# Kernel optimization log

Measured on AMD Instinct MI355X. Metric: run time of the kernel, lower is better.

Reference implementation:

```python
import jax, jax.numpy as jnp
import numpy as np

WIN = 8     # sliding-chunk window size (Long2DSCSelfAttention default w=8)
HEADS = 8   # num_heads


def setup_inputs() -> dict:
    key = jax.random.key(0)
    ks = jax.random.split(key, 3)
    B, C, H, W = 4, 512, 64, 64
    x = jax.random.normal(ks[0], (B, C, H, W), jnp.float32)
    w_qkv = jax.random.normal(ks[1], (3 * C, C), jnp.float32) * 0.02
    b_qkv = jnp.zeros((3 * C,), jnp.float32)
    w_proj = jax.random.normal(ks[2], (C, C), jnp.float32) * 0.02
    b_proj = jnp.zeros((C,), jnp.float32)
    return {"x": x, "w_qkv": w_qkv, "b_qkv": b_qkv, "w_proj": w_proj, "b_proj": b_proj}


def _chunk(t, nh, nw, win):
    B, _, _, h, d = t.shape
    t = t.reshape(B, nh, win, nw, win, h, d)
    return t.transpose(0, 5, 1, 3, 2, 4, 6).reshape(B, h, nh, nw, win * win, d)


def reference(x, w_qkv, b_qkv, w_proj, b_proj):
    B, C, H, W = x.shape
    win, heads = WIN, HEADS
    d = C // heads
    nh, nw = H // win, W // win
    m = win * win  # tokens per chunk

    xf = x.transpose(0, 2, 3, 1)                      # [B,H,W,C]
    qkv = xf @ w_qkv.T + b_qkv                        # [B,H,W,3C]
    qkv = qkv.reshape(B, H, W, 3, heads, d)
    q = _chunk(qkv[..., 0, :, :], nh, nw, win)        # [B,h,nh,nw,m,d]
    k = _chunk(qkv[..., 1, :, :], nh, nw, win)
    v = _chunk(qkv[..., 2, :, :], nh, nw, win)

    # pad chunk grid by one chunk on each side; gather 3x3 chunk neighborhoods
    kp = jnp.pad(k, ((0, 0), (0, 0), (1, 1), (1, 1), (0, 0), (0, 0)))
    vp = jnp.pad(v, ((0, 0), (0, 0), (1, 1), (1, 1), (0, 0), (0, 0)))
    k9 = jnp.concatenate([kp[:, :, i:i + nh, j:j + nw] for i in range(3) for j in range(3)], axis=4)  # [B,h,nh,nw,9m,d]
    v9 = jnp.concatenate([vp[:, :, i:i + nh, j:j + nw] for i in range(3) for j in range(3)], axis=4)

    # validity mask for neighbor chunks at the image boundary
    valid = jnp.pad(jnp.ones((nh, nw), bool), ((1, 1), (1, 1)))
    vmask = jnp.concatenate(
        [jnp.repeat(valid[i:i + nh, j:j + nw][..., None], m, axis=-1) for i in range(3) for j in range(3)],
        axis=-1)                                      # [nh,nw,9m]

    scale = float(d) ** -0.5
    attn = jnp.einsum('bhxyqd,bhxykd->bhxyqk', q * scale, k9)      # [B,h,nh,nw,m,9m]
    neg = jnp.asarray(-1e9, attn.dtype)
    attn = jnp.where(vmask[None, None, :, :, None, :], attn, neg)
    attn = jax.nn.softmax(attn, axis=-1)
    out = jnp.einsum('bhxyqk,bhxykd->bhxyqd', attn, v9)            # [B,h,nh,nw,m,d]

    out = out.reshape(B, heads, nh, nw, win, win, d)
    out = out.transpose(0, 2, 4, 3, 5, 1, 6).reshape(B, H, W, C)
    out = out @ w_proj.T + b_proj
    return out.transpose(0, 3, 1, 2)                               # [B,C,H,W]
```

## Files before the change

kernel.cpp:

```cpp
#include <hip/hip_runtime.h>
#include <cstdint>
#include <cstddef>

namespace {

constexpr int kC = 512;
constexpr int kHW = 4096;
constexpr int kHeads = 8;
constexpr int kChunkElems = 64 * 64;

typedef float f32x4 __attribute__((ext_vector_type(4)));
typedef _Float16 f16x8 __attribute__((ext_vector_type(8)));
union FragU { uint4 u; f16x8 h; };

__device__ __forceinline__ ushort f16rn(float x) {
  _Float16 h = (_Float16)x;
  ushort u;
  __builtin_memcpy(&u, &h, 2);
  return u;
}
__device__ __forceinline__ uint pack2(ushort a, ushort b) {
  return (uint)a | ((uint)b << 16);
}
__device__ __forceinline__ float fexp2(float x) {
  return exp2f(x);
}
__device__ __forceinline__ uint pkrtz(float a, float b) {
  auto h = __builtin_amdgcn_cvt_pkrtz(a, b);
  uint u;
  __builtin_memcpy(&u, &h, 4);
  return u;
}
__device__ __forceinline__ void gld16(const void* g, void* lds) {
  __builtin_amdgcn_global_load_lds(
      (const __attribute__((address_space(1))) uint32_t*)g,
      (__attribute__((address_space(3))) uint32_t*)lds, 16, 0, 0);
}

__global__ __launch_bounds__(256)
void convw16_kernel(const float* __restrict__ wqkv, ushort* __restrict__ wqh,
                    const float* __restrict__ wproj, ushort* __restrict__ wph)
{
  const int bx = blockIdx.x;
  const float* src;
  ushort* dst;
  int idx;
  if (bx < 384) { src = wqkv; dst = wqh; idx = (bx * 256 + threadIdx.x) * 8; }
  else { src = wproj; dst = wph; idx = ((bx - 384) * 256 + threadIdx.x) * 8; }
  float4 v0 = *(const float4*)(src + idx);
  float4 v1 = *(const float4*)(src + idx + 4);
  float xs[8] = {v0.x, v0.y, v0.z, v0.w, v1.x, v1.y, v1.z, v1.w};
  ushort hh[8];
#pragma unroll
  for (int e = 0; e < 8; ++e) hh[e] = f16rn(xs[e]);
  *(uint4*)(dst + idx) = make_uint4(pack2(hh[0], hh[1]), pack2(hh[2], hh[3]),
                                    pack2(hh[4], hh[5]), pack2(hh[6], hh[7]));
}

__global__ __launch_bounds__(256)
void convx_kernel(const float* __restrict__ x, ushort* __restrict__ xt)
{
  __shared__ float LT[64][68];
  const int tid = threadIdx.x;
  const int t0 = blockIdx.x * 64;
  const int c0 = blockIdx.y * 64;
  const int b  = blockIdx.z;
  const float* xb = x + (size_t)b * kC * kHW;

#pragma unroll
  for (int u = 0; u < 4; ++u) {
    int idx = tid + u * 256;
    int rc = idx >> 4;
    int t4 = (idx & 15) << 2;
    float4 val = *(const float4*)(xb + (size_t)(c0 + rc) * kHW + t0 + t4);
    LT[t4 + 0][rc] = val.x;
    LT[t4 + 1][rc] = val.y;
    LT[t4 + 2][rc] = val.z;
    LT[t4 + 3][rc] = val.w;
  }
  __syncthreads();
#pragma unroll
  for (int u = 0; u < 4; ++u) {
    int idx = tid + u * 256;
    int rt = idx >> 4;
    int c4 = (idx & 15) << 2;
    float4 v = *(const float4*)&LT[rt][c4];
    size_t o = ((size_t)b * kHW + t0 + rt) * kC + c0 + c4;
    *(ushort4*)(xt + o) = make_ushort4(f16rn(v.x), f16rn(v.y),
                                       f16rn(v.z), f16rn(v.w));
  }
}

__global__ __launch_bounds__(256)
void qkv_mfma_kernel(const ushort* __restrict__ xt,
                     const ushort* __restrict__ wq,
                     const float* __restrict__ bqkv,
                     ushort* __restrict__ qo, ushort* __restrict__ ko,
                     ushort* __restrict__ vo)
{
  __shared__ __align__(16) ushort As[128 * 64];
  __shared__ __align__(16) ushort Bs[128 * 64];

  const int tid  = threadIdx.x;
  const int lane = tid & 63;
  const int wv   = tid >> 6;
  const int quad = lane >> 4;
  const int l15  = lane & 15;
  const int wm = wv & 1, wn = wv >> 1;
  const int m0 = blockIdx.x * 128;
  const int n0 = blockIdx.y * 128;
  const int b  = blockIdx.z;

  const ushort* xb = xt + (size_t)b * kHW * kC;

  auto stage = [&](int k0) {
#pragma unroll
    for (int ii = 0; ii < 4; ++ii) {
      int i = wv * 4 + ii;
      int m = i * 8 + (lane >> 3);
      int gch = (lane & 7) ^ (m & 7);
      gld16(xb + (size_t)(m0 + m) * kC + k0 + gch * 8, (char*)As + i * 1024);
      gld16(wq + (size_t)(n0 + m) * kC + k0 + gch * 8, (char*)Bs + i * 1024);
    }
  };

  f32x4 acc[4][4];
#pragma unroll
  for (int i = 0; i < 4; ++i)
#pragma unroll
    for (int j = 0; j < 4; ++j) acc[i][j] = (f32x4){0.f, 0.f, 0.f, 0.f};

  stage(0);

  for (int kt = 0; kt < 8; ++kt) {
    asm volatile("s_waitcnt vmcnt(0)" ::: "memory");
    asm volatile("s_barrier" ::: "memory");

    FragU a0[4], a1[4], b0[4], b1[4];
#pragma unroll
    for (int mi = 0; mi < 4; ++mi) {
      int mr = wm * 64 + mi * 16 + l15;
      int sw = mr & 7;
      a0[mi].u = *(const uint4*)&As[mr * 64 + ((quad ^ sw) * 8)];
      a1[mi].u = *(const uint4*)&As[mr * 64 + (((4 + quad) ^ sw) * 8)];
    }
#pragma unroll
    for (int ni = 0; ni < 4; ++ni) {
      int nr = wn * 64 + ni * 16 + l15;
      int sw = nr & 7;
      b0[ni].u = *(const uint4*)&Bs[nr * 64 + ((quad ^ sw) * 8)];
      b1[ni].u = *(const uint4*)&Bs[nr * 64 + (((4 + quad) ^ sw) * 8)];
    }
    asm volatile("s_waitcnt lgkmcnt(0)" ::: "memory");
    asm volatile("s_barrier" ::: "memory");

    if (kt < 7) stage((kt + 1) * 64);

#pragma unroll
    for (int mi = 0; mi < 4; ++mi)
#pragma unroll
      for (int ni = 0; ni < 4; ++ni)
        acc[mi][ni] = __builtin_amdgcn_mfma_f32_16x16x32_f16(a0[mi].h, b0[ni].h, acc[mi][ni], 0, 0, 0);
#pragma unroll
    for (int mi = 0; mi < 4; ++mi)
#pragma unroll
      for (int ni = 0; ni < 4; ++ni)
        acc[mi][ni] = __builtin_amdgcn_mfma_f32_16x16x32_f16(a1[mi].h, b1[ni].h, acc[mi][ni], 0, 0, 0);
  }

  const int sec = n0 >> 9;
  const int jwbase = n0 + wn * 64;
  const int head = (jwbase >> 6) & 7;
  const size_t hbb = ((size_t)b * kHeads + head) * 64;
  float biasv[4];
#pragma unroll
  for (int ni = 0; ni < 4; ++ni) biasv[ni] = bqkv[jwbase + ni * 16 + l15];

  if (sec == 2) {
#pragma unroll
    for (int ni = 0; ni < 4; ++ni) {
      int dd = ni * 16 + l15;
#pragma unroll
      for (int mi = 0; mi < 4; ++mi) {
        int t0t = m0 + wm * 64 + mi * 16 + quad * 4;
        int h = t0t >> 6, w = t0t & 63;
        int cy = h >> 3, iy = h & 7, cx = w >> 3, ix = w & 7;
        size_t cb = (hbb + cy * 8 + cx) * (size_t)kChunkElems;
        int tokb = iy * 8 + ix;
        ushort hh[4];
#pragma unroll
        for (int r = 0; r < 4; ++r) hh[r] = f16rn(acc[mi][ni][r] + biasv[ni]);
        *(ushort4*)(vo + cb + (size_t)dd * 64 + tokb) = make_ushort4(hh[0], hh[1], hh[2], hh[3]);
      }
    }
  } else {
    ushort* dst = (sec == 0) ? qo : ko;
    const float sc = (sec == 0) ? 0.125f * 1.44269504089f : 1.0f;
    ushort* tH = As + wv * 1152;
    const int ltok = lane >> 2;
    const int dd0 = (lane & 3) * 16;
#pragma unroll
    for (int mi = 0; mi < 4; ++mi) {
#pragma unroll
      for (int ni = 0; ni < 4; ++ni)
#pragma unroll
        for (int r = 0; r < 4; ++r)
          tH[(quad * 4 + r) * 68 + ni * 16 + l15] =
              f16rn((acc[mi][ni][r] + biasv[ni]) * sc);
      int tg = m0 + wm * 64 + mi * 16 + ltok;
      int h = tg >> 6, w = tg & 63;
      int cy = h >> 3, iy = h & 7, cx = w >> 3, ix = w & 7;
      size_t cb = (hbb + cy * 8 + cx) * (size_t)kChunkElems
                + (size_t)(iy * 8 + ix) * 64 + dd0;
      uint4 h0 = *(const uint4*)&tH[ltok * 68 + dd0];
      uint4 h1 = *(const uint4*)&tH[ltok * 68 + dd0 + 8];
      *(uint4*)(dst + cb) = h0;
      *(uint4*)(dst + cb + 8) = h1;
    }
  }
}

__global__ __launch_bounds__(256)
void attn_mfma_kernel(const ushort* __restrict__ qg, const ushort* __restrict__ kg,
                      const ushort* __restrict__ vg,
                      ushort* __restrict__ ao)
{
  __shared__ __align__(16) ushort KB[4096], VB[4096];
  __shared__ __align__(16) ushort Ps[4 * 16 * 72];

  const int tid  = threadIdx.x;
  const int lane = tid & 63;
  const int wv   = tid >> 6;
  const int quad = lane >> 4;
  const int l15  = lane & 15;

  const int bx = blockIdx.x;
  const int g  = (bx & 7) * 4 + ((bx >> 3) >> 6);
  const int c  = (bx >> 3) & 63;
  const int b = g >> 3, head = g & 7;
  const int cy = c >> 3, cx = c & 7;

  const size_t hb = (size_t)b * kHeads + head;
  const size_t gbase = hb * 64 * (size_t)kChunkElems;
  const size_t cbase = gbase + (size_t)c * (size_t)kChunkElems;

  FragU aQ0, aQ1;
  {
    const ushort* qr = qg + cbase + (size_t)(wv * 16 + l15) * 64 + quad * 8;
    aQ0.u = *(const uint4*)(qr);
    aQ1.u = *(const uint4*)(qr + 32);
  }

  const int boff = ((lane >> 3) * 64) + (((lane & 7) ^ (lane >> 3)) * 8);
  const ushort* kgB = kg + gbase + boff + (size_t)(wv * 2) * 512;
  const ushort* vgB = vg + gbase + boff + (size_t)(wv * 2) * 512;
  char* kDst0 = (char*)KB + (wv * 2) * 1024;
  char* vDst0 = (char*)VB + (wv * 2) * 1024;

  int kvOff0[4], kvOff1[4];
  {
    const int sw = l15 & 7;
#pragma unroll
    for (int nt = 0; nt < 4; ++nt) {
      int row = nt * 16 + l15;
      kvOff0[nt] = row * 64 + ((quad ^ sw) * 8);
      kvOff1[nt] = row * 64 + (((4 + quad) ^ sw) * 8);
    }
  }

  ushort* PsW = Ps + wv * 1152;
  ushort* pWr = PsW + l15 * 72 + quad * 4;
  const ushort* pRd = PsW + l15 * 72 + quad * 8;

  unsigned long long list = 0ull;
  int cnt = 0;
#pragma unroll
  for (int p = 0; p < 9; ++p) {
    const int dy = p / 3 - 1, dx = p % 3 - 1;
    int ny = cy + dy, nx = cx + dx;
    if ((unsigned)ny < 8u && (unsigned)nx < 8u) {
      list |= (unsigned long long)(ny * 8 + nx) << (6 * cnt);
      ++cnt;
    }
  }

  f32x4 o[4];
#pragma unroll
  for (int r = 0; r < 4; ++r) o[r] = (f32x4){0.f, 0.f, 0.f, 0.f};
  float rsum = 0.f;

  {
    int ch0 = (int)(list & 63);
    const ushort* pk = kgB + (size_t)ch0 * kChunkElems;
    gld16(pk, kDst0);
    gld16(pk + 512, kDst0 + 1024);
    const ushort* pv = vgB + (size_t)ch0 * kChunkElems;
    gld16(pv, vDst0);
    gld16(pv + 512, vDst0 + 1024);
  }

  for (int i = 0; i < cnt; ++i) {
    const bool more = (i + 1 < cnt);
    const int chn = (int)((list >> (6 * (i + 1))) & 63);

    asm volatile("s_waitcnt vmcnt(2)" ::: "memory");
    asm volatile("s_barrier" ::: "memory");

    FragU kf[8];
#pragma unroll
    for (int nt = 0; nt < 4; ++nt) {
      kf[nt * 2].u     = *(const uint4*)&KB[kvOff0[nt]];
      kf[nt * 2 + 1].u = *(const uint4*)&KB[kvOff1[nt]];
    }
    asm volatile("s_waitcnt lgkmcnt(0)" ::: "memory");
    asm volatile("s_waitcnt vmcnt(0)" ::: "memory");
    asm volatile("s_barrier" ::: "memory");

    if (more) {
      const ushort* pk = kgB + (size_t)chn * kChunkElems;
      gld16(pk, kDst0);
      gld16(pk + 512, kDst0 + 1024);
    }

    f32x4 s[4];
#pragma unroll
    for (int nt = 0; nt < 4; ++nt) s[nt] = (f32x4){0.f, 0.f, 0.f, 0.f};
#pragma unroll
    for (int nt = 0; nt < 4; ++nt) {
      s[nt] = __builtin_amdgcn_mfma_f32_16x16x32_f16(kf[nt * 2].h, aQ0.h, s[nt], 0, 0, 0);
      s[nt] = __builtin_amdgcn_mfma_f32_16x16x32_f16(kf[nt * 2 + 1].h, aQ1.h, s[nt], 0, 0, 0);
    }

#pragma unroll
    for (int nt = 0; nt < 4; ++nt) {
      float e0 = fexp2(s[nt][0]);
      float e1 = fexp2(s[nt][1]);
      float e2 = fexp2(s[nt][2]);
      float e3 = fexp2(s[nt][3]);
      rsum += (e0 + e1) + (e2 + e3);
      *(uint2*)(pWr + nt * 16) = make_uint2(pkrtz(e0, e1), pkrtz(e2, e3));
    }

    FragU aP0, aP1;
    aP0.u = *(const uint4*)(pRd);
    aP1.u = *(const uint4*)(pRd + 32);

#pragma unroll
    for (int nt = 0; nt < 4; ++nt) {
      FragU v0, v1;
      v0.u = *(const uint4*)&VB[kvOff0[nt]];
      v1.u = *(const uint4*)&VB[kvOff1[nt]];
      o[nt] = __builtin_amdgcn_mfma_f32_16x16x32_f16(v0.h, aP0.h, o[nt], 0, 0, 0);
      o[nt] = __builtin_amdgcn_mfma_f32_16x16x32_f16(v1.h, aP1.h, o[nt], 0, 0, 0);
    }

    asm volatile("s_waitcnt lgkmcnt(0)" ::: "memory");
    asm volatile("s_barrier" ::: "memory");
    if (more) {
      const ushort* pv = vgB + (size_t)chn * kChunkElems;
      gld16(pv, vDst0);
      gld16(pv + 512, vDst0 + 1024);
    }
  }

  rsum += __shfl_xor(rsum, 16, 64);
  rsum += __shfl_xor(rsum, 32, 64);
  const float inv = 1.0f / rsum;

  const int trg = wv * 16 + l15;
  const int hp = cy * 8 + (trg >> 3);
  const int wp = cx * 8 + (trg & 7);
  const size_t obase = ((size_t)b * kHW + hp * 64 + wp) * (size_t)kC + head * 64;

#pragma unroll
  for (int nt = 0; nt < 4; ++nt) {
    float v0 = o[nt][0] * inv;
    float v1 = o[nt][1] * inv;
    float v2 = o[nt][2] * inv;
    float v3 = o[nt][3] * inv;
    *(ushort4*)(ao + obase + nt * 16 + quad * 4) =
        make_ushort4(f16rn(v0), f16rn(v1), f16rn(v2), f16rn(v3));
  }
}

__global__ __launch_bounds__(256)
void proj_mfma_kernel(const ushort* __restrict__ ao,
                      const ushort* __restrict__ wp,
                      const float* __restrict__ bproj,
                      float* __restrict__ out)
{
  __shared__ __align__(16) ushort As[128 * 64];
  __shared__ __align__(16) ushort Bs[128 * 64];

  const int tid  = threadIdx.x;
  const int lane = tid & 63;
  const int wv   = tid >> 6;
  const int quad = lane >> 4;
  const int l15  = lane & 15;
  const int wm = wv & 1, wn = wv >> 1;
  const int n0g = blockIdx.x * 128;
  const int m0  = blockIdx.y * 128;
  const int b   = n0g >> 12;
  const int tl0 = n0g & 4095;

  auto stage = [&](int k0) {
#pragma unroll
    for (int ii = 0; ii < 4; ++ii) {
      int i = wv * 4 + ii;
      int m = i * 8 + (lane >> 3);
      int gch = (lane & 7) ^ (m & 7);
      gld16(wp + (size_t)(m0 + m) * kC + k0 + gch * 8, (char*)As + i * 1024);
      gld16(ao + (size_t)(n0g + m) * kC + k0 + gch * 8, (char*)Bs + i * 1024);
    }
  };

  f32x4 acc[4][4];
#pragma unroll
  for (int i = 0; i < 4; ++i)
#pragma unroll
    for (int j = 0; j < 4; ++j) acc[i][j] = (f32x4){0.f, 0.f, 0.f, 0.f};

  stage(0);

  for (int kt = 0; kt < 8; ++kt) {
    asm volatile("s_waitcnt vmcnt(0)" ::: "memory");
    asm volatile("s_barrier" ::: "memory");

    FragU a0[4], a1[4], b0[4], b1[4];
#pragma unroll
    for (int mi = 0; mi < 4; ++mi) {
      int mr = wm * 64 + mi * 16 + l15;
      int sw = mr & 7;
      a0[mi].u = *(const uint4*)&As[mr * 64 + ((quad ^ sw) * 8)];
      a1[mi].u = *(const uint4*)&As[mr * 64 + (((4 + quad) ^ sw) * 8)];
    }
#pragma unroll
    for (int ni = 0; ni < 4; ++ni) {
      int nr = wn * 64 + ni * 16 + l15;
      int sw = nr & 7;
      b0[ni].u = *(const uint4*)&Bs[nr * 64 + ((quad ^ sw) * 8)];
      b1[ni].u = *(const uint4*)&Bs[nr * 64 + (((4 + quad) ^ sw) * 8)];
    }
    asm volatile("s_waitcnt lgkmcnt(0)" ::: "memory");
    asm volatile("s_barrier" ::: "memory");

    if (kt < 7) stage((kt + 1) * 64);

#pragma unroll
    for (int mi = 0; mi < 4; ++mi)
#pragma unroll
      for (int ni = 0; ni < 4; ++ni)
        acc[mi][ni] = __builtin_amdgcn_mfma_f32_16x16x32_f16(a0[mi].h, b0[ni].h, acc[mi][ni], 0, 0, 0);
#pragma unroll
    for (int mi = 0; mi < 4; ++mi)
#pragma unroll
      for (int ni = 0; ni < 4; ++ni)
        acc[mi][ni] = __builtin_amdgcn_mfma_f32_16x16x32_f16(a1[mi].h, b1[ni].h, acc[mi][ni], 0, 0, 0);
  }

#pragma unroll
  for (int mi = 0; mi < 4; ++mi)
#pragma unroll
    for (int r = 0; r < 4; ++r) {
      int c = m0 + wm * 64 + mi * 16 + quad * 4 + r;
      float bias = bproj[c];
      size_t rowb = ((size_t)b * kC + c) * (size_t)kHW + tl0 + wn * 64;
#pragma unroll
      for (int ni = 0; ni < 4; ++ni)
        out[rowb + ni * 16 + l15] = acc[mi][ni][r] + bias;
    }
}

}

extern "C" void kernel_launch(void* const* d_in, const int* in_sizes, int n_in,
                              void* d_out, int out_size, void* d_ws, size_t ws_size,
                              hipStream_t stream)
{
  const float* x     = (const float*)d_in[0];
  const float* wqkv  = (const float*)d_in[1];
  const float* bqkv  = (const float*)d_in[2];
  const float* wproj = (const float*)d_in[3];
  const float* bproj = (const float*)d_in[4];
  float* out = (float*)d_out;

  const size_t seg = (size_t)2048 * kChunkElems;
  ushort* base = (ushort*)d_ws;
  ushort* qb = base + 0 * seg;
  ushort* kb = base + 1 * seg;
  ushort* vb = base + 2 * seg;
  ushort* xt = base + 3 * seg;
  ushort* ao = xt;
  ushort* wp16 = base + 4 * seg;
  ushort* wqh = base + 5 * seg;

  convw16_kernel<<<dim3(512), 256, 0, stream>>>(wqkv, wqh, wproj, wp16);
  convx_kernel<<<dim3(64, 8, 4), 256, 0, stream>>>(x, xt);
  qkv_mfma_kernel<<<dim3(32, 12, 4), 256, 0, stream>>>(xt, wqh, bqkv,
                                                       qb, kb, vb);
  attn_mfma_kernel<<<dim3(2048), 256, 0, stream>>>(qb, kb, vb, ao);
  proj_mfma_kernel<<<dim3(128, 4), 256, 0, stream>>>(ao, wp16, bproj, out);
}
```

Measured before the change: 176.9 us.

## Switch attention kernel to 32x32x16 MFMA tiles with 2x2 wave split

Reworks the attention kernel so each wave computes a 32-query by 32-key tile with 32x32x16 MFMA instructions instead of 16x16x32, splitting waves across query and key halves. P is shared through a block-wide LDS buffer and needs an extra barrier each chunk, and row sums are combined across waves through a small LDS array at the end. This halves the K fragment loads per wave and uses fewer, larger MFMAs, at the cost of added synchronisation and cross-wave dependencies in the P·V stage.

```diff
diff --git a/kernel.cpp b/kernel.cpp
--- a/kernel.cpp
+++ b/kernel.cpp
@@ -10,6 +10,7 @@
 constexpr int kChunkElems = 64 * 64;
 
 typedef float f32x4 __attribute__((ext_vector_type(4)));
+typedef float f32x16 __attribute__((ext_vector_type(16)));
 typedef _Float16 f16x8 __attribute__((ext_vector_type(8)));
 union FragU { uint4 u; f16x8 h; };
 
@@ -226,13 +227,16 @@
                       ushort* __restrict__ ao)
 {
   __shared__ __align__(16) ushort KB[4096], VB[4096];
-  __shared__ __align__(16) ushort Ps[4 * 16 * 72];
+  __shared__ __align__(16) ushort Ps[64 * 72];
+  __shared__ __align__(16) float  RsF[128];
 
   const int tid  = threadIdx.x;
   const int lane = tid & 63;
   const int wv   = tid >> 6;
-  const int quad = lane >> 4;
-  const int l15  = lane & 15;
+  const int l31  = lane & 31;
+  const int hi   = lane >> 5;
+  const int kq   = wv & 1;
+  const int qq   = wv >> 1;
 
   const int bx = blockIdx.x;
   const int g  = (bx & 7) * 4 + ((bx >> 3) >> 6);
@@ -244,11 +248,11 @@
   const size_t gbase = hb * 64 * (size_t)kChunkElems;
   const size_t cbase = gbase + (size_t)c * (size_t)kChunkElems;
 
-  FragU aQ0, aQ1;
+  FragU qf[4];
   {
-    const ushort* qr = qg + cbase + (size_t)(wv * 16 + l15) * 64 + quad * 8;
-    aQ0.u = *(const uint4*)(qr);
-    aQ1.u = *(const uint4*)(qr + 32);
+    const ushort* qr = qg + cbase + (size_t)(qq * 32 + l31) * 64 + hi * 8;
+#pragma unroll
+    for (int s = 0; s < 4; ++s) qf[s].u = *(const uint4*)(qr + s * 16);
   }
 
   const int boff = ((lane >> 3) * 64) + (((lane & 7) ^ (lane >> 3)) * 8);
@@ -257,20 +261,17 @@
   char* kDst0 = (char*)KB + (wv * 2) * 1024;
   char* vDst0 = (char*)VB + (wv * 2) * 1024;
 
-  int kvOff0[4], kvOff1[4];
+  int kvOff[4];
   {
-    const int sw = l15 & 7;
-#pragma unroll
-    for (int nt = 0; nt < 4; ++nt) {
-      int row = nt * 16 + l15;
-      kvOff0[nt] = row * 64 + ((quad ^ sw) * 8);
-      kvOff1[nt] = row * 64 + (((4 + quad) ^ sw) * 8);
-    }
-  }
-
-  ushort* PsW = Ps + wv * 1152;
-  ushort* pWr = PsW + l15 * 72 + quad * 4;
-  const ushort* pRd = PsW + l15 * 72 + quad * 8;
+    const int row = kq * 32 + l31;
+    const int sw = l31 & 7;
+#pragma unroll
+    for (int s = 0; s < 4; ++s)
+      kvOff[s] = row * 64 + (((2 * s + hi) ^ sw) * 8);
+  }
+
+  ushort* pWr = Ps + (qq * 32 + l31) * 72 + kq * 32 + 4 * hi;
+  const ushort* pRd = Ps + (qq * 32 + l31) * 72 + hi * 8;
 
   unsigned long long list = 0ull;
   int cnt = 0;
@@ -284,9 +285,9 @@
     }
   }
 
-  f32x4 o[4];
-#pragma unroll
-  for (int r = 0; r < 4; ++r) o[r] = (f32x4){0.f, 0.f, 0.f, 0.f};
+  f32x16 o32;
+#pragma unroll
+  for (int r = 0; r < 16; ++r) o32[r] = 0.f;
   float rsum = 0.f;
 
   {
@@ -306,12 +307,9 @@
     asm volatile("s_waitcnt vmcnt(2)" ::: "memory");
     asm volatile("s_barrier" ::: "memory");
 
-    FragU kf[8];
-#pragma unroll
-    for (int nt = 0; nt < 4; ++nt) {
-      kf[nt * 2].u     = *(const uint4*)&KB[kvOff0[nt]];
-      kf[nt * 2 + 1].u = *(const uint4*)&KB[kvOff1[nt]];
-    }
+    FragU kf[4];
+#pragma unroll
+    for (int s = 0; s < 4; ++s) kf[s].u = *(const uint4*)&KB[kvOff[s]];
     asm volatile("s_waitcnt lgkmcnt(0)" ::: "memory");
     asm volatile("s_waitcnt vmcnt(0)" ::: "memory");
     asm volatile("s_barrier" ::: "memory");
@@ -322,36 +320,32 @@
       gld16(pk + 512, kDst0 + 1024);
     }
 
-    f32x4 s[4];
-#pragma unroll
-    for (int nt = 0; nt < 4; ++nt) s[nt] = (f32x4){0.f, 0.f, 0.f, 0.f};
-#pragma unroll
-    for (int nt = 0; nt < 4; ++nt) {
-      s[nt] = __builtin_amdgcn_mfma_f32_16x16x32_f16(kf[nt * 2].h, aQ0.h, s[nt], 0, 0, 0);
-      s[nt] = __builtin_amdgcn_mfma_f32_16x16x32_f16(kf[nt * 2 + 1].h, aQ1.h, s[nt], 0, 0, 0);
-    }
-
-#pragma unroll
-    for (int nt = 0; nt < 4; ++nt) {
-      float e0 = fexp2(s[nt][0]);
-      float e1 = fexp2(s[nt][1]);
-      float e2 = fexp2(s[nt][2]);
-      float e3 = fexp2(s[nt][3]);
-      rsum += (e0 + e1) + (e2 + e3);
-      *(uint2*)(pWr + nt * 16) = make_uint2(pkrtz(e0, e1), pkrtz(e2, e3));
-    }
-
-    FragU aP0, aP1;
-    aP0.u = *(const uint4*)(pRd);
-    aP1.u = *(const uint4*)(pRd + 32);
-
-#pragma unroll
-    for (int nt = 0; nt < 4; ++nt) {
-      FragU v0, v1;
-      v0.u = *(const uint4*)&VB[kvOff0[nt]];
-      v1.u = *(const uint4*)&VB[kvOff1[nt]];
-      o[nt] = __builtin_amdgcn_mfma_f32_16x16x32_f16(v0.h, aP0.h, o[nt], 0, 0, 0);
-      o[nt] = __builtin_amdgcn_mfma_f32_16x16x32_f16(v1.h, aP1.h, o[nt], 0, 0, 0);
+    f32x16 s32;
+#pragma unroll
+    for (int r = 0; r < 16; ++r) s32[r] = 0.f;
+#pragma unroll
+    for (int s = 0; s < 4; ++s)
+      s32 = __builtin_amdgcn_mfma_f32_32x32x16_f16(kf[s].h, qf[s].h, s32, 0, 0, 0);
+
+    float e[16];
+#pragma unroll
+    for (int r = 0; r < 16; ++r) e[r] = fexp2(s32[r]);
+#pragma unroll
+    for (int r = 0; r < 16; ++r) rsum += e[r];
+#pragma unroll
+    for (int gg = 0; gg < 4; ++gg)
+      *(uint2*)(pWr + gg * 8) =
+          make_uint2(pkrtz(e[4 * gg], e[4 * gg + 1]),
+                     pkrtz(e[4 * gg + 2], e[4 * gg + 3]));
+    asm volatile("s_waitcnt lgkmcnt(0)" ::: "memory");
+    asm volatile("s_barrier" ::: "memory");
+
+#pragma unroll
+    for (int s = 0; s < 4; ++s) {
+      FragU vf, pf;
+      vf.u = *(const uint4*)&VB[kvOff[s]];
+      pf.u = *(const uint4*)(pRd + s * 16);
+      o32 = __builtin_amdgcn_mfma_f32_32x32x16_f16(vf.h, pf.h, o32, 0, 0, 0);
     }
 
     asm volatile("s_waitcnt lgkmcnt(0)" ::: "memory");
@@ -363,23 +357,26 @@
     }
   }
 
-  rsum += __shfl_xor(rsum, 16, 64);
   rsum += __shfl_xor(rsum, 32, 64);
-  const float inv = 1.0f / rsum;
-
-  const int trg = wv * 16 + l15;
-  const int hp = cy * 8 + (trg >> 3);
-  const int wp = cx * 8 + (trg & 7);
-  const size_t obase = ((size_t)b * kHW + hp * 64 + wp) * (size_t)kC + head * 64;
-
-#pragma unroll
-  for (int nt = 0; nt < 4; ++nt) {
-    float v0 = o[nt][0] * inv;
-    float v1 = o[nt][1] * inv;
-    float v2 = o[nt][2] * inv;
-    float v3 = o[nt][3] * inv;
-    *(ushort4*)(ao + obase + nt * 16 + quad * 4) =
-        make_ushort4(f16rn(v0), f16rn(v1), f16rn(v2), f16rn(v3));
+  if (lane < 32) RsF[kq * 64 + qq * 32 + lane] = rsum;
+  asm volatile("s_waitcnt lgkmcnt(0)" ::: "memory");
+  asm volatile("s_barrier" ::: "memory");
+  const float tot = RsF[qq * 32 + l31] + RsF[64 + qq * 32 + l31];
+  const float inv = 1.0f / tot;
+
+  const int tok = qq * 32 + l31;
+  const int hp = cy * 8 + (tok >> 3);
+  const int wp = cx * 8 + (tok & 7);
+  const size_t obase = ((size_t)b * kHW + hp * 64 + wp) * (size_t)kC
+                     + head * 64 + kq * 32 + 4 * hi;
+
+#pragma unroll
+  for (int gg = 0; gg < 4; ++gg) {
+    ushort4 hh = make_ushort4(f16rn(o32[4 * gg + 0] * inv),
+                              f16rn(o32[4 * gg + 1] * inv),
+                              f16rn(o32[4 * gg + 2] * inv),
+                              f16rn(o32[4 * gg + 3] * inv));
+    *(ushort4*)(ao + obase + gg * 8) = hh;
   }
 }
 
```

Result: slower. 184.2 us (+4.1%).
